# Kernel tuning notes

Hardware: AMD Instinct MI355X
Metric: run time of the kernel (lower is better)

Reference implementation:

```python
import jax, jax.numpy as jnp
import numpy as np

B, S, D, H, C = 8, 4096, 1024, 256, 512
INIT_RANGE = 0.01

def setup_inputs() -> dict:
    key = jax.random.key(0)
    ks = jax.random.split(key, 6)
    return {
        "hidden_states": jax.random.normal(ks[0], (B, S, D), dtype=jnp.float32),
        "conditions": jax.random.normal(ks[1], (B, C), dtype=jnp.float32),
        "down_project": jax.random.normal(ks[2], (D, H), dtype=jnp.float32) * INIT_RANGE,
        "down_gamma": jax.random.normal(ks[3], (C, H), dtype=jnp.float32),
        "down_beta": jnp.zeros((C, H), dtype=jnp.float32),
        "up_project": jax.random.normal(ks[4], (H, D), dtype=jnp.float32) * INIT_RANGE,
        "up_gamma": jax.random.normal(ks[5], (C, D), dtype=jnp.float32),
        "up_beta": jnp.zeros((C, D), dtype=jnp.float32),
    }

def reference(hidden_states, conditions, down_project, down_gamma, down_beta,
              up_project, up_gamma, up_beta):
    # per-example modulation coefficients: [B, H] / [B, D]
    dg = conditions @ down_gamma   # [B, H]
    db = conditions @ down_beta    # [B, H]
    ug = conditions @ up_gamma     # [B, D]
    ub = conditions @ up_beta      # [B, D]
    # per-example down weight: W_down * gamma (column scale) + beta (added to every row)
    w_down = down_project[None, :, :] * dg[:, None, :] + db[:, None, :]  # [B, D, H]
    down = jnp.einsum('bsd,bdh->bsh', hidden_states, w_down)             # [B, S, H]
    act = jax.nn.relu(down)
    w_up = up_project[None, :, :] * ug[:, None, :] + ub[:, None, :]      # [B, H, D]
    up = jnp.einsum('bsh,bhd->bsd', act, w_up)                           # [B, S, D]
    # (the original computes self.ln(up) but discards the result)
    return up + hidden_states
```

## Files before the change

kernel.cpp:

```cpp
#include <hip/hip_runtime.h>
#include <hip/hip_bf16.h>

typedef __attribute__((ext_vector_type(4))) float f32x4;
typedef __attribute__((ext_vector_type(8))) short s16x8;
typedef __attribute__((ext_vector_type(8))) unsigned short u16x8;
typedef __attribute__((ext_vector_type(4))) unsigned int u32x4;

#define DEVFN static __device__ __forceinline__

DEVFN unsigned short f2bf(float f) {
  union { float f; unsigned int u; } v; v.f = f;
  unsigned int u = v.u;
  u += 0x7fffu + ((u >> 16) & 1u);
  return (unsigned short)(u >> 16);
}

DEVFN unsigned int cvt_pk(float a, float b) {
  __hip_bfloat162 h = __float22bfloat162_rn(make_float2(a, b));
  union { __hip_bfloat162 h; unsigned int u; } v; v.h = h; return v.u;
}

DEVFN void gl_lds16(const void* g, void* l) {
  __builtin_amdgcn_global_load_lds((__attribute__((address_space(1))) void*)g,
                                   (__attribute__((address_space(3))) void*)l, 16, 0, 0);
}

#define SB() __builtin_amdgcn_sched_barrier(0)
#define VMW(n) asm volatile("s_waitcnt vmcnt(" #n ")" ::: "memory")
#define LGKM0() asm volatile("s_waitcnt lgkmcnt(0)" ::: "memory")
#define BAR() { SB(); __builtin_amdgcn_s_barrier(); SB(); }

#define DG_OFF 0
#define DB_OFF 2048
#define UG_OFF 4096
#define UB_OFF 12288
#define W1_BYTE 81920
#define W2_BYTE 606208

__global__ void prep_kernel(const float* __restrict__ cond,
                            const float* __restrict__ dgm, const float* __restrict__ dbt,
                            const float* __restrict__ ugm, const float* __restrict__ ubt,
                            const float* __restrict__ Wd, const float* __restrict__ Wu,
                            char* __restrict__ ws) {
  __shared__ float lc[4096];
  __shared__ float red[2048];
  const int t = threadIdx.x;

  if (blockIdx.x < 32) {
    const int ks = blockIdx.x;
    const int n = t;
    const float* sp = Wd + (size_t)(ks * 32) * 256 + n;
    unsigned short tmp[32];
#pragma unroll
    for (int kk = 0; kk < 32; ++kk) tmp[kk] = f2bf(sp[(size_t)kk * 256]);
    char* dst = ws + W1_BYTE + (size_t)ks * 16384 + n * 64;
#pragma unroll
    for (int g = 0; g < 4; ++g) {
      u16x8 v;
#pragma unroll
      for (int e = 0; e < 8; ++e) v[e] = tmp[g * 8 + e];
      *(u16x8*)(dst + ((g ^ ((n >> 1) & 3)) << 4)) = v;
    }
    return;
  }
  if (blockIdx.x < 64) {
    int b2 = blockIdx.x - 32;
    int ntile = b2 >> 2, kc = b2 & 3;
    const int n = t >> 1, kh = t & 1;
    const float* sp = Wu + (size_t)(kc * 64 + kh * 32) * 1024 + ntile * 128 + n;
    unsigned short tmp[32];
#pragma unroll
    for (int kk = 0; kk < 32; ++kk) tmp[kk] = f2bf(sp[(size_t)kk * 1024]);
    char* dst = ws + W2_BYTE + (size_t)(ntile * 4 + kc) * 16384 + n * 128;
#pragma unroll
    for (int gi = 0; gi < 4; ++gi) {
      u16x8 v;
#pragma unroll
      for (int e = 0; e < 8; ++e) v[e] = tmp[gi * 8 + e];
      int g = kh * 4 + gi;
      *(u16x8*)(dst + ((g ^ (n & 7)) << 4)) = v;
    }
    return;
  }

  float* coef = (float*)ws;
#pragma unroll
  for (int i = 0; i < 16; ++i) lc[t + i * 256] = cond[t + i * 256];
  __syncthreads();
  const int bid2 = blockIdx.x - 64;
  const int col = bid2 * 16 + (t & 15);
  const int ks = t >> 4;
  const float* src; int ncol, cl;
  if (col < 256)       { src = dgm; ncol = 256;  cl = col; }
  else if (col < 512)  { src = dbt; ncol = 256;  cl = col - 256; }
  else if (col < 1536) { src = ugm; ncol = 1024; cl = col - 512; }
  else                 { src = ubt; ncol = 1024; cl = col - 1536; }
  float acc[8] = {};
  for (int k = ks * 32; k < ks * 32 + 32; ++k) {
    float g = src[(size_t)k * ncol + cl];
#pragma unroll
    for (int b = 0; b < 8; ++b) acc[b] = fmaf(lc[b * 512 + k], g, acc[b]);
  }
#pragma unroll
  for (int b = 0; b < 8; ++b) red[(ks * 16 + (t & 15)) * 8 + b] = acc[b];
  __syncthreads();
  if (t < 128) {
    int c = t >> 3, b = t & 7;
    float s = 0.f;
#pragma unroll
    for (int k2 = 0; k2 < 16; ++k2) s += red[(k2 * 16 + c) * 8 + b];
    int colg = bid2 * 16 + c;
    float* dst; int ncol2, cl2;
    if (colg < 256)       { dst = coef + DG_OFF; ncol2 = 256;  cl2 = colg; }
    else if (colg < 512)  { dst = coef + DB_OFF; ncol2 = 256;  cl2 = colg - 256; }
    else if (colg < 1536) { dst = coef + UG_OFF; ncol2 = 1024; cl2 = colg - 512; }
    else                  { dst = coef + UB_OFF; ncol2 = 1024; cl2 = colg - 1536; }
    dst[b * ncol2 + cl2] = s;
  }
}

__global__ __launch_bounds__(512, 4)
void fused_kernel(const float* __restrict__ X, char* __restrict__ ws,
                  float* __restrict__ out) {
  __shared__ char lds[81920];
  const int tid = threadIdx.x;
  const int lane = tid & 63, lr = lane & 15, lq = lane >> 4;
  const int wave = tid >> 6;
  const int wm = wave >> 2, wn = wave & 3;

  const int raw = blockIdx.x;
  const int m = (raw & 7) * 64 + (raw >> 3);
  const int row0 = m << 6;
  const int b = m >> 6;

  const float* coef = (const float*)ws;
  const char* w1 = ws + W1_BYTE;
  const char* w2 = ws + W2_BYTE;

  const int srow = tid >> 4, sg = tid & 15;
  const float* xsrc = X + (size_t)(row0 + srow) * 1024 + ((sg ^ (srow & 15)) << 2);

  int aoff[2][2][2];
#pragma unroll
  for (int mf = 0; mf < 2; ++mf)
#pragma unroll
    for (int h = 0; h < 2; ++h) {
      int r = wm * 32 + mf * 16 + lr;
      int g0 = h * 8 + lq * 2;
      aoff[mf][h][0] = r * 256 + ((g0 ^ (r & 15)) << 4);
      aoff[mf][h][1] = r * 256 + (((g0 + 1) ^ (r & 15)) << 4);
    }
  int boff[4];
#pragma unroll
  for (int nf = 0; nf < 4; ++nf) {
    int n = wn * 64 + nf * 16 + lr;
    boff[nf] = n * 64 + ((lq ^ ((n >> 1) & 3)) << 4);
  }

  f32x4 acc1[2][4] = {};
  float hacc[2] = {0.f, 0.f};

#define XB(i) (lds + 32768 + (i) * 16384)
#define W1B   (lds + 65536)
#define STAGE_X(t)                                                               \
  { char* xb = XB((t) & 1);                                                      \
    gl_lds16(xsrc + (size_t)(t) * 64, xb + tid * 16);                            \
    gl_lds16(xsrc + 32 * 1024 + (size_t)(t) * 64, xb + 8192 + tid * 16); }
#define STAGE_W1(ks)                                                             \
  { gl_lds16(w1 + (size_t)(ks) * 16384 + tid * 16, W1B + tid * 16);              \
    gl_lds16(w1 + (size_t)(ks) * 16384 + 8192 + tid * 16, W1B + 8192 + tid * 16); }

#define MFMA_SUB(Xc, h)                                                          \
  { s16x8 afr[2];                                                                \
    _Pragma("unroll")                                                            \
    for (int mf = 0; mf < 2; ++mf) {                                             \
      f32x4 fa0 = *(const f32x4*)((Xc) + aoff[mf][h][0]);                        \
      f32x4 fa1 = *(const f32x4*)((Xc) + aoff[mf][h][1]);                        \
      if (wn == 0)                                                               \
        hacc[mf] += fa0[0] + fa0[1] + fa0[2] + fa0[3] +                          \
                    fa1[0] + fa1[1] + fa1[2] + fa1[3];                           \
      union { u32x4 u; s16x8 s; } cv;                                            \
      cv.u[0] = cvt_pk(fa0[0], fa0[1]); cv.u[1] = cvt_pk(fa0[2], fa0[3]);        \
      cv.u[2] = cvt_pk(fa1[0], fa1[1]); cv.u[3] = cvt_pk(fa1[2], fa1[3]);        \
      afr[mf] = cv.s;                                                            \
    }                                                                            \
    s16x8 bfr[4];                                                                \
    _Pragma("unroll")                                                            \
    for (int nf = 0; nf < 4; ++nf) bfr[nf] = *(const s16x8*)(W1B + boff[nf]);    \
    _Pragma("unroll")                                                            \
    for (int mf = 0; mf < 2; ++mf)                                               \
      _Pragma("unroll")                                                          \
      for (int nf = 0; nf < 4; ++nf)                                             \
        acc1[mf][nf] = __builtin_amdgcn_mfma_f32_16x16x32_bf16(afr[mf], bfr[nf], \
                                                               acc1[mf][nf], 0, 0, 0); }

  STAGE_X(0); STAGE_X(1); STAGE_W1(0);
  VMW(0); BAR();

  for (int t = 0; t < 16; ++t) {
    const char* Xc = XB(t & 1);
    MFMA_SUB(Xc, 0);
    LGKM0(); BAR();
    STAGE_W1(2 * t + 1);
    VMW(0); BAR();
    MFMA_SUB(Xc, 1);
    LGKM0(); BAR();
    if (t < 15) STAGE_W1(2 * t + 2);
    if (t < 14) { STAGE_X(t + 2); VMW(2); }
    else        { VMW(0); }
    BAR();
  }

  float* hsumb = (float*)(lds + 32768);
  float* asp   = (float*)(lds + 33024);
  if (wn == 0) {
#pragma unroll
    for (int mf = 0; mf < 2; ++mf) {
      float s = hacc[mf];
      s += __shfl_xor(s, 16); s += __shfl_xor(s, 32);
      if (lq == 0) hsumb[wm * 32 + mf * 16 + lr] = s;
    }
  }
  __syncthreads();

  float dgv[4], dbv[4];
#pragma unroll
  for (int nf = 0; nf < 4; ++nf) {
    int h = wn * 64 + nf * 16 + lr;
    dgv[nf] = coef[DG_OFF + b * 256 + h];
    dbv[nf] = coef[DB_OFF + b * 256 + h];
  }

  float asacc[2][4] = {};
#pragma unroll
  for (int nf = 0; nf < 4; ++nf) {
    int g = nf * 2 + (lr >> 3);
    char* nbase = lds + wn * 8192 + (lr & 7) * 2;
    float dg_ = dgv[nf], db_ = dbv[nf];
#pragma unroll
    for (int mf = 0; mf < 2; ++mf) {
#pragma unroll
      for (int j = 0; j < 4; ++j) {
        int r = wm * 32 + mf * 16 + lq * 4 + j;
        float v = acc1[mf][nf][j] * dg_ + db_ * hsumb[r];
        v = fmaxf(v, 0.f);
        asacc[mf][j] += v;
        *(unsigned short*)(nbase + r * 128 + ((g ^ (r & 7)) << 4)) = f2bf(v);
      }
    }
  }
#pragma unroll
  for (int mf = 0; mf < 2; ++mf)
#pragma unroll
    for (int j = 0; j < 4; ++j) {
      float s = asacc[mf][j];
      s += __shfl_xor(s, 1); s += __shfl_xor(s, 2); s += __shfl_xor(s, 4); s += __shfl_xor(s, 8);
      if (lr == 0) asp[wn * 64 + wm * 32 + mf * 16 + lq * 4 + j] = s;
    }
  __syncthreads();

  float asv[2][4];
#pragma unroll
  for (int mf = 0; mf < 2; ++mf)
#pragma unroll
    for (int j = 0; j < 4; ++j) {
      int r = wm * 32 + mf * 16 + lq * 4 + j;
      asv[mf][j] = asp[r] + asp[64 + r] + asp[128 + r] + asp[192 + r];
    }
  __syncthreads();

  int a2off[2][2], b2off[2][2];
#pragma unroll
  for (int mf = 0; mf < 2; ++mf)
#pragma unroll
    for (int kf = 0; kf < 2; ++kf) {
      int r = wm * 32 + mf * 16 + lr;
      a2off[mf][kf] = r * 128 + (((kf * 4 + lq) ^ (r & 7)) << 4);
    }
#pragma unroll
  for (int nf = 0; nf < 2; ++nf)
#pragma unroll
    for (int kf = 0; kf < 2; ++kf) {
      int nl = wn * 32 + nf * 16 + lr;
      b2off[nf][kf] = nl * 128 + (((kf * 4 + lq) ^ (nl & 7)) << 4);
    }

#define W2B(s) (lds + 32768 + ((s) % 3) * 16384)
#define STAGE_W2(s)                                                              \
  { gl_lds16(w2 + (size_t)(s) * 16384 + tid * 16, W2B(s) + tid * 16);            \
    gl_lds16(w2 + (size_t)(s) * 16384 + 8192 + tid * 16,                         \
             W2B(s) + 8192 + tid * 16); }

  STAGE_W2(0); STAGE_W2(1);
  VMW(2); BAR();

  float ugv[2], ubv[2];
#pragma unroll
  for (int s = 0; s < 32; ++s) {
    const int nt = s >> 2, kc = s & 3;
    f32x4 acc2[2][2];
    if (kc == 0) {
#pragma unroll
      for (int mf = 0; mf < 2; ++mf)
#pragma unroll
        for (int nf = 0; nf < 2; ++nf) acc2[mf][nf] = (f32x4){0.f, 0.f, 0.f, 0.f};
    }
    static f32x4 dummy;
    const char* Wb = W2B(s);
#pragma unroll
    for (int kf = 0; kf < 2; ++kf) {
      s16x8 a2[2], bb[2];
#pragma unroll
      for (int mf = 0; mf < 2; ++mf)
        a2[mf] = *(const s16x8*)(lds + kc * 8192 + a2off[mf][kf]);
#pragma unroll
      for (int nf = 0; nf < 2; ++nf)
        bb[nf] = *(const s16x8*)(Wb + b2off[nf][kf]);
#pragma unroll
      for (int mf = 0; mf < 2; ++mf)
#pragma unroll
        for (int nf = 0; nf < 2; ++nf)
          acc2[mf][nf] = __builtin_amdgcn_mfma_f32_16x16x32_bf16(a2[mf], bb[nf], acc2[mf][nf], 0, 0, 0);
    }
    LGKM0(); BAR();

    if (kc == 0) {
#pragma unroll
      for (int nf = 0; nf < 2; ++nf) {
        int d = nt * 128 + wn * 32 + nf * 16 + lr;
        ugv[nf] = coef[UG_OFF + b * 1024 + d];
        ubv[nf] = coef[UB_OFF + b * 1024 + d];
      }
    }
    if (s + 2 < 32) STAGE_W2(s + 2);
    if (kc == 3) {
#pragma unroll
      for (int mf = 0; mf < 2; ++mf)
#pragma unroll
        for (int j = 0; j < 4; ++j) {
          int r = wm * 32 + mf * 16 + lq * 4 + j;
          size_t gbase = (size_t)(row0 + r) * 1024 + nt * 128 + wn * 32;
#pragma unroll
          for (int nf = 0; nf < 2; ++nf) {
            size_t gi = gbase + nf * 16 + lr;
            out[gi] = acc2[mf][nf][j] * ugv[nf] + ubv[nf] * asv[mf][j] + X[gi];
          }
        }
    }
    if (s < 31) {
      if (s + 2 >= 32)  { VMW(0); }
      else if (kc == 3) { VMW(16); }
      else              { VMW(2); }
      BAR();
    }
    (void)dummy;
  }
}

extern "C" void kernel_launch(void* const* d_in, const int* in_sizes, int n_in,
                              void* d_out, int out_size, void* d_ws, size_t ws_size,
                              hipStream_t stream) {
  const float* hidden       = (const float*)d_in[0];
  const float* conditions   = (const float*)d_in[1];
  const float* down_project = (const float*)d_in[2];
  const float* down_gamma   = (const float*)d_in[3];
  const float* down_beta    = (const float*)d_in[4];
  const float* up_project   = (const float*)d_in[5];
  const float* up_gamma     = (const float*)d_in[6];
  const float* up_beta      = (const float*)d_in[7];
  float* out = (float*)d_out;
  char* ws = (char*)d_ws;

  prep_kernel<<<224, 256, 0, stream>>>(conditions, down_gamma, down_beta, up_gamma, up_beta,
                                       down_project, up_project, ws);
  fused_kernel<<<512, 512, 0, stream>>>(hidden, ws, out);
}
```

Measured before the change: 89.42 us.

## Load X directly to registers and triple-buffer W1 in first GEMM

Phase one now reads X straight into registers through inline-asm global loads, double-buffered two steps ahead, instead of staging it through LDS. The wave grid is remapped to 4x2, so each wave covers 16 rows by 128 columns. W1 tiles go into a three-slot LDS ring with one barrier per K-step instead of four. Phase two preloads all up-gamma/beta coefficients up front and drops one barrier per step by relaxing the vmcnt waits. The aim is to cut LDS traffic and barrier stalls. The cost is more register pressure and fragile hand-counted vmcnt values that mix with the inline-asm loads.

```diff
diff --git a/kernel.cpp b/kernel.cpp
--- a/kernel.cpp
+++ b/kernel.cpp
@@ -23,6 +23,15 @@
 DEVFN void gl_lds16(const void* g, void* l) {
   __builtin_amdgcn_global_load_lds((__attribute__((address_space(1))) void*)g,
                                    (__attribute__((address_space(3))) void*)l, 16, 0, 0);
+}
+
+DEVFN f32x4 async_ld4(const float* p) {
+  f32x4 v;
+  asm volatile("global_load_dwordx4 %0, %1, off"
+               : "=v"(v)
+               : "v"((unsigned long long)(uintptr_t)p)
+               : "memory");
+  return v;
 }
 
 #define SB() __builtin_amdgcn_sched_barrier(0)
@@ -126,7 +135,8 @@
   const int tid = threadIdx.x;
   const int lane = tid & 63, lr = lane & 15, lq = lane >> 4;
   const int wave = tid >> 6;
-  const int wm = wave >> 2, wn = wave & 3;
+  const int wm1 = wave >> 1, wn1 = wave & 1;
+  const int wm2 = wave >> 2, wn2 = wave & 3;
 
   const int raw = blockIdx.x;
   const int m = (raw & 7) * 64 + (raw >> 3);
@@ -137,151 +147,133 @@
   const char* w1 = ws + W1_BYTE;
   const char* w2 = ws + W2_BYTE;
 
-  const int srow = tid >> 4, sg = tid & 15;
-  const float* xsrc = X + (size_t)(row0 + srow) * 1024 + ((sg ^ (srow & 15)) << 2);
-
-  int aoff[2][2][2];
-#pragma unroll
-  for (int mf = 0; mf < 2; ++mf)
-#pragma unroll
-    for (int h = 0; h < 2; ++h) {
-      int r = wm * 32 + mf * 16 + lr;
-      int g0 = h * 8 + lq * 2;
-      aoff[mf][h][0] = r * 256 + ((g0 ^ (r & 15)) << 4);
-      aoff[mf][h][1] = r * 256 + (((g0 + 1) ^ (r & 15)) << 4);
-    }
-  int boff[4];
-#pragma unroll
-  for (int nf = 0; nf < 4; ++nf) {
-    int n = wn * 64 + nf * 16 + lr;
+  const float* xrow = X + (size_t)(row0 + wm1 * 16 + lr) * 1024 + lq * 8;
+
+  int boff[8];
+#pragma unroll
+  for (int nf = 0; nf < 8; ++nf) {
+    int n = wn1 * 128 + nf * 16 + lr;
     boff[nf] = n * 64 + ((lq ^ ((n >> 1) & 3)) << 4);
   }
 
-  f32x4 acc1[2][4] = {};
-  float hacc[2] = {0.f, 0.f};
-
-#define XB(i) (lds + 32768 + (i) * 16384)
-#define W1B   (lds + 65536)
-#define STAGE_X(t)                                                               \
-  { char* xb = XB((t) & 1);                                                      \
-    gl_lds16(xsrc + (size_t)(t) * 64, xb + tid * 16);                            \
-    gl_lds16(xsrc + 32 * 1024 + (size_t)(t) * 64, xb + 8192 + tid * 16); }
+  f32x4 acc1[8] = {};
+  float hacc = 0.f;
+  f32x4 xvA[2], xvB[2];
+
+#define XLOAD(BUF, t)                                                            \
+  { BUF[0] = async_ld4(xrow + (size_t)(t) * 32);                                 \
+    BUF[1] = async_ld4(xrow + (size_t)(t) * 32 + 4); }
 #define STAGE_W1(ks)                                                             \
-  { gl_lds16(w1 + (size_t)(ks) * 16384 + tid * 16, W1B + tid * 16);              \
-    gl_lds16(w1 + (size_t)(ks) * 16384 + 8192 + tid * 16, W1B + 8192 + tid * 16); }
-
-#define MFMA_SUB(Xc, h)                                                          \
-  { s16x8 afr[2];                                                                \
+  { char* dst = lds + 32768 + ((ks) % 3) * 16384;                                \
+    gl_lds16(w1 + (size_t)(ks) * 16384 + tid * 16, dst + tid * 16);              \
+    gl_lds16(w1 + (size_t)(ks) * 16384 + 8192 + tid * 16, dst + 8192 + tid * 16); }
+
+#define P1_STEP(t, BUF)                                                          \
+  { s16x8 afr;                                                                   \
+    { if (wn1 == 0)                                                              \
+        hacc += BUF[0][0] + BUF[0][1] + BUF[0][2] + BUF[0][3] +                  \
+                BUF[1][0] + BUF[1][1] + BUF[1][2] + BUF[1][3];                   \
+      union { u32x4 u; s16x8 s; } cv;                                            \
+      cv.u[0] = cvt_pk(BUF[0][0], BUF[0][1]);                                    \
+      cv.u[1] = cvt_pk(BUF[0][2], BUF[0][3]);                                    \
+      cv.u[2] = cvt_pk(BUF[1][0], BUF[1][1]);                                    \
+      cv.u[3] = cvt_pk(BUF[1][2], BUF[1][3]);                                    \
+      afr = cv.s; }                                                              \
+    if ((t) < 30) XLOAD(BUF, (t) + 2);                                           \
+    const char* Wb = lds + 32768 + ((t) % 3) * 16384;                            \
+    s16x8 bfr[8];                                                                \
     _Pragma("unroll")                                                            \
-    for (int mf = 0; mf < 2; ++mf) {                                             \
-      f32x4 fa0 = *(const f32x4*)((Xc) + aoff[mf][h][0]);                        \
-      f32x4 fa1 = *(const f32x4*)((Xc) + aoff[mf][h][1]);                        \
-      if (wn == 0)                                                               \
-        hacc[mf] += fa0[0] + fa0[1] + fa0[2] + fa0[3] +                          \
-                    fa1[0] + fa1[1] + fa1[2] + fa1[3];                           \
-      union { u32x4 u; s16x8 s; } cv;                                            \
-      cv.u[0] = cvt_pk(fa0[0], fa0[1]); cv.u[1] = cvt_pk(fa0[2], fa0[3]);        \
-      cv.u[2] = cvt_pk(fa1[0], fa1[1]); cv.u[3] = cvt_pk(fa1[2], fa1[3]);        \
-      afr[mf] = cv.s;                                                            \
-    }                                                                            \
-    s16x8 bfr[4];                                                                \
+    for (int nf = 0; nf < 8; ++nf) bfr[nf] = *(const s16x8*)(Wb + boff[nf]);     \
     _Pragma("unroll")                                                            \
-    for (int nf = 0; nf < 4; ++nf) bfr[nf] = *(const s16x8*)(W1B + boff[nf]);    \
-    _Pragma("unroll")                                                            \
-    for (int mf = 0; mf < 2; ++mf)                                               \
-      _Pragma("unroll")                                                          \
-      for (int nf = 0; nf < 4; ++nf)                                             \
-        acc1[mf][nf] = __builtin_amdgcn_mfma_f32_16x16x32_bf16(afr[mf], bfr[nf], \
-                                                               acc1[mf][nf], 0, 0, 0); }
-
-  STAGE_X(0); STAGE_X(1); STAGE_W1(0);
-  VMW(0); BAR();
-
-  for (int t = 0; t < 16; ++t) {
-    const char* Xc = XB(t & 1);
-    MFMA_SUB(Xc, 0);
-    LGKM0(); BAR();
-    STAGE_W1(2 * t + 1);
-    VMW(0); BAR();
-    MFMA_SUB(Xc, 1);
-    LGKM0(); BAR();
-    if (t < 15) STAGE_W1(2 * t + 2);
-    if (t < 14) { STAGE_X(t + 2); VMW(2); }
-    else        { VMW(0); }
-    BAR();
+    for (int nf = 0; nf < 8; ++nf)                                               \
+      acc1[nf] = __builtin_amdgcn_mfma_f32_16x16x32_bf16(afr, bfr[nf],           \
+                                                         acc1[nf], 0, 0, 0);     \
+    LGKM0(); SB();                                                               \
+    if ((t) < 30) { STAGE_W1((t) + 2); VMW(4); }                                 \
+    else if ((t) == 30) { VMW(0); }                                              \
+    BAR(); }
+
+  XLOAD(xvA, 0); STAGE_W1(0);
+  XLOAD(xvB, 1); STAGE_W1(1);
+  VMW(4); BAR();
+
+#pragma unroll
+  for (int t2 = 0; t2 < 16; ++t2) {
+    P1_STEP(2 * t2, xvA);
+    P1_STEP(2 * t2 + 1, xvB);
   }
 
   float* hsumb = (float*)(lds + 32768);
   float* asp   = (float*)(lds + 33024);
-  if (wn == 0) {
-#pragma unroll
-    for (int mf = 0; mf < 2; ++mf) {
-      float s = hacc[mf];
-      s += __shfl_xor(s, 16); s += __shfl_xor(s, 32);
-      if (lq == 0) hsumb[wm * 32 + mf * 16 + lr] = s;
-    }
-  }
-  __syncthreads();
-
-  float dgv[4], dbv[4];
-#pragma unroll
-  for (int nf = 0; nf < 4; ++nf) {
-    int h = wn * 64 + nf * 16 + lr;
-    dgv[nf] = coef[DG_OFF + b * 256 + h];
-    dbv[nf] = coef[DB_OFF + b * 256 + h];
-  }
-
-  float asacc[2][4] = {};
-#pragma unroll
-  for (int nf = 0; nf < 4; ++nf) {
-    int g = nf * 2 + (lr >> 3);
-    char* nbase = lds + wn * 8192 + (lr & 7) * 2;
-    float dg_ = dgv[nf], db_ = dbv[nf];
-#pragma unroll
-    for (int mf = 0; mf < 2; ++mf) {
-#pragma unroll
-      for (int j = 0; j < 4; ++j) {
-        int r = wm * 32 + mf * 16 + lq * 4 + j;
-        float v = acc1[mf][nf][j] * dg_ + db_ * hsumb[r];
-        v = fmaxf(v, 0.f);
-        asacc[mf][j] += v;
-        *(unsigned short*)(nbase + r * 128 + ((g ^ (r & 7)) << 4)) = f2bf(v);
-      }
-    }
-  }
+  __syncthreads();
+  if (wn1 == 0) {
+    float s = hacc;
+    s += __shfl_xor(s, 16); s += __shfl_xor(s, 32);
+    if (lq == 0) hsumb[wm1 * 16 + lr] = s;
+  }
+  __syncthreads();
+
+  float asacc[4] = {};
+#pragma unroll
+  for (int nf = 0; nf < 8; ++nf) {
+    int h = wn1 * 128 + nf * 16 + lr;
+    float dg_ = coef[DG_OFF + b * 256 + h];
+    float db_ = coef[DB_OFF + b * 256 + h];
+    int kc = h >> 6, kl = h & 63;
+    char* nbase = lds + kc * 8192 + (kl >> 3 << 4 ? 0 : 0);
+    int g = kl >> 3;
+    char* base = lds + kc * 8192 + (kl & 7) * 2;
+#pragma unroll
+    for (int j = 0; j < 4; ++j) {
+      int r = wm1 * 16 + lq * 4 + j;
+      float v = acc1[nf][j] * dg_ + db_ * hsumb[r];
+      v = fmaxf(v, 0.f);
+      asacc[j] += v;
+      *(unsigned short*)(base + r * 128 + ((g ^ (r & 7)) << 4)) = f2bf(v);
+    }
+    (void)nbase;
+  }
+#pragma unroll
+  for (int j = 0; j < 4; ++j) {
+    float s = asacc[j];
+    s += __shfl_xor(s, 1); s += __shfl_xor(s, 2); s += __shfl_xor(s, 4); s += __shfl_xor(s, 8);
+    if (lr == 0) asp[wave * 16 + lq * 4 + j] = s;
+  }
+  __syncthreads();
+
+  float asv[2][4];
 #pragma unroll
   for (int mf = 0; mf < 2; ++mf)
 #pragma unroll
     for (int j = 0; j < 4; ++j) {
-      float s = asacc[mf][j];
-      s += __shfl_xor(s, 1); s += __shfl_xor(s, 2); s += __shfl_xor(s, 4); s += __shfl_xor(s, 8);
-      if (lr == 0) asp[wn * 64 + wm * 32 + mf * 16 + lq * 4 + j] = s;
-    }
-  __syncthreads();
-
-  float asv[2][4];
+      int r2 = wm2 * 32 + mf * 16 + lq * 4 + j;
+      asv[mf][j] = asp[(r2 >> 4) * 32 + (r2 & 15)] + asp[(r2 >> 4) * 32 + 16 + (r2 & 15)];
+    }
+  __syncthreads();
+
+  float ugA[8][2], ubA[8][2];
+#pragma unroll
+  for (int nt = 0; nt < 8; ++nt)
+#pragma unroll
+    for (int nf = 0; nf < 2; ++nf) {
+      int d = nt * 128 + wn2 * 32 + nf * 16 + lr;
+      ugA[nt][nf] = coef[UG_OFF + b * 1024 + d];
+      ubA[nt][nf] = coef[UB_OFF + b * 1024 + d];
+    }
+
+  int a2off[2][2], b2off[2][2];
 #pragma unroll
   for (int mf = 0; mf < 2; ++mf)
 #pragma unroll
-    for (int j = 0; j < 4; ++j) {
-      int r = wm * 32 + mf * 16 + lq * 4 + j;
-      asv[mf][j] = asp[r] + asp[64 + r] + asp[128 + r] + asp[192 + r];
-    }
-  __syncthreads();
-
-  int a2off[2][2], b2off[2][2];
-#pragma unroll
-  for (int mf = 0; mf < 2; ++mf)
-#pragma unroll
     for (int kf = 0; kf < 2; ++kf) {
-      int r = wm * 32 + mf * 16 + lr;
+      int r = wm2 * 32 + mf * 16 + lr;
       a2off[mf][kf] = r * 128 + (((kf * 4 + lq) ^ (r & 7)) << 4);
     }
 #pragma unroll
   for (int nf = 0; nf < 2; ++nf)
 #pragma unroll
     for (int kf = 0; kf < 2; ++kf) {
-      int nl = wn * 32 + nf * 16 + lr;
+      int nl = wn2 * 32 + nf * 16 + lr;
       b2off[nf][kf] = nl * 128 + (((kf * 4 + lq) ^ (nl & 7)) << 4);
     }
 
@@ -294,18 +286,16 @@
   STAGE_W2(0); STAGE_W2(1);
   VMW(2); BAR();
 
-  float ugv[2], ubv[2];
+  f32x4 acc2[2][2];
 #pragma unroll
   for (int s = 0; s < 32; ++s) {
     const int nt = s >> 2, kc = s & 3;
-    f32x4 acc2[2][2];
     if (kc == 0) {
 #pragma unroll
       for (int mf = 0; mf < 2; ++mf)
 #pragma unroll
         for (int nf = 0; nf < 2; ++nf) acc2[mf][nf] = (f32x4){0.f, 0.f, 0.f, 0.f};
     }
-    static f32x4 dummy;
     const char* Wb = W2B(s);
 #pragma unroll
     for (int kf = 0; kf < 2; ++kf) {
@@ -322,38 +312,32 @@
         for (int nf = 0; nf < 2; ++nf)
           acc2[mf][nf] = __builtin_amdgcn_mfma_f32_16x16x32_bf16(a2[mf], bb[nf], acc2[mf][nf], 0, 0, 0);
     }
-    LGKM0(); BAR();
-
-    if (kc == 0) {
-#pragma unroll
-      for (int nf = 0; nf < 2; ++nf) {
-        int d = nt * 128 + wn * 32 + nf * 16 + lr;
-        ugv[nf] = coef[UG_OFF + b * 1024 + d];
-        ubv[nf] = coef[UB_OFF + b * 1024 + d];
-      }
-    }
+    LGKM0(); SB();
+
     if (s + 2 < 32) STAGE_W2(s + 2);
+    SB();
     if (kc == 3) {
 #pragma unroll
       for (int mf = 0; mf < 2; ++mf)
 #pragma unroll
         for (int j = 0; j < 4; ++j) {
-          int r = wm * 32 + mf * 16 + lq * 4 + j;
-          size_t gbase = (size_t)(row0 + r) * 1024 + nt * 128 + wn * 32;
+          int r = wm2 * 32 + mf * 16 + lq * 4 + j;
+          size_t gbase = (size_t)(row0 + r) * 1024 + nt * 128 + wn2 * 32;
 #pragma unroll
           for (int nf = 0; nf < 2; ++nf) {
             size_t gi = gbase + nf * 16 + lr;
-            out[gi] = acc2[mf][nf][j] * ugv[nf] + ubv[nf] * asv[mf][j] + X[gi];
+            out[gi] = acc2[mf][nf][j] * ugA[nt][nf] + ubA[nt][nf] * asv[mf][j] + X[gi];
           }
         }
+      SB();
     }
     if (s < 31) {
-      if (s + 2 >= 32)  { VMW(0); }
-      else if (kc == 3) { VMW(16); }
-      else              { VMW(2); }
+      if (s == 30)            { VMW(0); }
+      else if (kc == 1 || kc == 2) { VMW(2); }
+      else if (s == 0)        { VMW(2); }
+      else                    { VMW(34); }
       BAR();
     }
-    (void)dummy;
   }
 }
 
```

Result: slower. 95.05 us (+6.3%).

## Triple-buffer W1 and prefetch two stages ahead in down-projection loop

Applied to the files above, without the earlier changes.

Restructures the first GEMM's main loop from a half-step scheme with one W1 buffer and four barriers per X tile into a 32-step loop. W1 is triple-buffered and prefetched two steps ahead, and X is double-buffered and issued at the start of each step. The LDS layout moves X to offset 0 and the W1 ring to 32K-80K. Each step now has one barrier with graded vmcnt waits, which is meant to hide global-to-LDS latency and cut synchronisation. It uses more LDS, and the loop is fully unrolled, which raises code size.

```diff
diff --git a/kernel.cpp b/kernel.cpp
--- a/kernel.cpp
+++ b/kernel.cpp
@@ -160,54 +160,54 @@
   f32x4 acc1[2][4] = {};
   float hacc[2] = {0.f, 0.f};
 
-#define XB(i) (lds + 32768 + (i) * 16384)
-#define W1B   (lds + 65536)
 #define STAGE_X(t)                                                               \
-  { char* xb = XB((t) & 1);                                                      \
+  { char* xb = lds + ((t) & 1) * 16384;                                          \
     gl_lds16(xsrc + (size_t)(t) * 64, xb + tid * 16);                            \
     gl_lds16(xsrc + 32 * 1024 + (size_t)(t) * 64, xb + 8192 + tid * 16); }
 #define STAGE_W1(ks)                                                             \
-  { gl_lds16(w1 + (size_t)(ks) * 16384 + tid * 16, W1B + tid * 16);              \
-    gl_lds16(w1 + (size_t)(ks) * 16384 + 8192 + tid * 16, W1B + 8192 + tid * 16); }
-
-#define MFMA_SUB(Xc, h)                                                          \
-  { s16x8 afr[2];                                                                \
-    _Pragma("unroll")                                                            \
-    for (int mf = 0; mf < 2; ++mf) {                                             \
-      f32x4 fa0 = *(const f32x4*)((Xc) + aoff[mf][h][0]);                        \
-      f32x4 fa1 = *(const f32x4*)((Xc) + aoff[mf][h][1]);                        \
-      if (wn == 0)                                                               \
-        hacc[mf] += fa0[0] + fa0[1] + fa0[2] + fa0[3] +                          \
-                    fa1[0] + fa1[1] + fa1[2] + fa1[3];                           \
-      union { u32x4 u; s16x8 s; } cv;                                            \
-      cv.u[0] = cvt_pk(fa0[0], fa0[1]); cv.u[1] = cvt_pk(fa0[2], fa0[3]);        \
-      cv.u[2] = cvt_pk(fa1[0], fa1[1]); cv.u[3] = cvt_pk(fa1[2], fa1[3]);        \
-      afr[mf] = cv.s;                                                            \
-    }                                                                            \
-    s16x8 bfr[4];                                                                \
-    _Pragma("unroll")                                                            \
-    for (int nf = 0; nf < 4; ++nf) bfr[nf] = *(const s16x8*)(W1B + boff[nf]);    \
-    _Pragma("unroll")                                                            \
-    for (int mf = 0; mf < 2; ++mf)                                               \
-      _Pragma("unroll")                                                          \
-      for (int nf = 0; nf < 4; ++nf)                                             \
-        acc1[mf][nf] = __builtin_amdgcn_mfma_f32_16x16x32_bf16(afr[mf], bfr[nf], \
-                                                               acc1[mf][nf], 0, 0, 0); }
-
-  STAGE_X(0); STAGE_X(1); STAGE_W1(0);
-  VMW(0); BAR();
-
-  for (int t = 0; t < 16; ++t) {
-    const char* Xc = XB(t & 1);
-    MFMA_SUB(Xc, 0);
-    LGKM0(); BAR();
-    STAGE_W1(2 * t + 1);
-    VMW(0); BAR();
-    MFMA_SUB(Xc, 1);
-    LGKM0(); BAR();
-    if (t < 15) STAGE_W1(2 * t + 2);
-    if (t < 14) { STAGE_X(t + 2); VMW(2); }
-    else        { VMW(0); }
+  { char* dst = lds + 32768 + ((ks) % 3) * 16384;                                \
+    gl_lds16(w1 + (size_t)(ks) * 16384 + tid * 16, dst + tid * 16);              \
+    gl_lds16(w1 + (size_t)(ks) * 16384 + 8192 + tid * 16, dst + 8192 + tid * 16); }
+
+  STAGE_W1(0); STAGE_X(0); STAGE_W1(1);
+  VMW(2); BAR();
+
+#pragma unroll
+  for (int s = 0; s < 32; ++s) {
+    if (s + 2 < 32) STAGE_W1(s + 2);
+    if ((s & 1) == 0 && (s >> 1) + 1 < 16) STAGE_X((s >> 1) + 1);
+    {
+      const char* Xc = lds + ((s >> 1) & 1) * 16384;
+      const char* Wb = lds + 32768 + (s % 3) * 16384;
+      const int h = s & 1;
+      s16x8 afr[2];
+#pragma unroll
+      for (int mf = 0; mf < 2; ++mf) {
+        f32x4 fa0 = *(const f32x4*)(Xc + aoff[mf][h][0]);
+        f32x4 fa1 = *(const f32x4*)(Xc + aoff[mf][h][1]);
+        if (wn == 0)
+          hacc[mf] += fa0[0] + fa0[1] + fa0[2] + fa0[3] +
+                      fa1[0] + fa1[1] + fa1[2] + fa1[3];
+        union { u32x4 u; s16x8 s_; } cv;
+        cv.u[0] = cvt_pk(fa0[0], fa0[1]); cv.u[1] = cvt_pk(fa0[2], fa0[3]);
+        cv.u[2] = cvt_pk(fa1[0], fa1[1]); cv.u[3] = cvt_pk(fa1[2], fa1[3]);
+        afr[mf] = cv.s_;
+      }
+      s16x8 bfr[4];
+#pragma unroll
+      for (int nf = 0; nf < 4; ++nf) bfr[nf] = *(const s16x8*)(Wb + boff[nf]);
+#pragma unroll
+      for (int mf = 0; mf < 2; ++mf)
+#pragma unroll
+        for (int nf = 0; nf < 4; ++nf)
+          acc1[mf][nf] = __builtin_amdgcn_mfma_f32_16x16x32_bf16(afr[mf], bfr[nf],
+                                                                 acc1[mf][nf], 0, 0, 0);
+    }
+    LGKM0(); SB();
+    if (s == 30)            { VMW(0); }
+    else if (s == 31)       { }
+    else if (s & 1)         { VMW(2); }
+    else                    { VMW(4); }
     BAR();
   }
 
@@ -305,7 +305,6 @@
 #pragma unroll
         for (int nf = 0; nf < 2; ++nf) acc2[mf][nf] = (f32x4){0.f, 0.f, 0.f, 0.f};
     }
-    static f32x4 dummy;
     const char* Wb = W2B(s);
 #pragma unroll
     for (int kf = 0; kf < 2; ++kf) {
@@ -353,7 +352,6 @@
       else              { VMW(2); }
       BAR();
     }
-    (void)dummy;
   }
 }
 
```

Measured after the change: 82.08 us. 1.09x faster.
